# Kernel optimization log

Hardware: AMD Instinct MI355X
Metric: run time of the kernel (lower is better)

Reference implementation:

```python
import jax, jax.numpy as jnp
import numpy as np

B, S, H, L = 64, 512, 768, 9


def setup_inputs() -> dict:
    key = jax.random.key(0)
    ks = jax.random.split(key, 8)
    hidden = jax.random.normal(ks[0], (B, S, H), jnp.float32)
    lengths = jax.random.randint(ks[1], (B,), S // 2, S + 1)
    attention_mask = (jnp.arange(S)[None, :] < lengths[:, None]).astype(jnp.int32)
    labels = jax.random.randint(ks[2], (B, S), 0, L)
    # sprinkle some -100 ignore labels like HF datasets do
    ignore = jax.random.uniform(ks[3], (B, S)) < 0.05
    labels = jnp.where(ignore, -100, labels)
    W = jax.random.normal(ks[4], (H, L), jnp.float32) * 0.02
    b = jnp.zeros((L,), jnp.float32)
    start_transitions = jax.random.uniform(ks[5], (L,), jnp.float32, -0.1, 0.1)
    end_transitions = jax.random.uniform(ks[6], (L,), jnp.float32, -0.1, 0.1)
    transitions = jax.random.uniform(ks[7], (L, L), jnp.float32, -0.1, 0.1)
    return dict(hidden=hidden, attention_mask=attention_mask, labels=labels, W=W, b=b,
                start_transitions=start_transitions, end_transitions=end_transitions,
                transitions=transitions)


def _crf_numerator(emissions, tags, maskf, start_t, end_t, trans):
    # score of the gold tag sequence (torchcrf _compute_score)
    first = start_t[tags[:, 0]] + jnp.take_along_axis(emissions[:, 0], tags[:, 0:1], axis=1)[:, 0]
    em = jnp.take_along_axis(emissions, tags[..., None], axis=2)[..., 0]      # [B,S]
    tr = trans[tags[:, :-1], tags[:, 1:]]                                     # [B,S-1]
    score = first + jnp.sum((em[:, 1:] + tr) * maskf[:, 1:], axis=1)
    last_idx = (jnp.sum(maskf, axis=1).astype(jnp.int32) - 1)
    last_tags = jnp.take_along_axis(tags, last_idx[:, None], axis=1)[:, 0]
    return score + end_t[last_tags]


def _crf_lognorm(emissions, maskf, start_t, end_t, trans):
    # forward algorithm (torchcrf _compute_normalizer) as a lax.scan
    score0 = start_t[None, :] + emissions[:, 0]                               # [B,L]
    em_seq = jnp.transpose(emissions[:, 1:], (1, 0, 2))                       # [S-1,B,L]
    m_seq = maskf[:, 1:].T                                                    # [S-1,B]

    def step(score, xs):
        em_t, m_t = xs
        nxt = jax.nn.logsumexp(score[:, :, None] + trans[None] + em_t[:, None, :], axis=1)
        return jnp.where(m_t[:, None] > 0, nxt, score), None

    score, _ = jax.lax.scan(step, score0, (em_seq, m_seq))
    return jax.nn.logsumexp(score + end_t[None, :], axis=1)


def _viterbi(emissions, maskf, start_t, end_t, trans):
    score0 = start_t[None, :] + emissions[:, 0]                               # [B,L]
    em_seq = jnp.transpose(emissions[:, 1:], (1, 0, 2))
    m_seq = maskf[:, 1:].T

    def step(score, xs):
        em_t, m_t = xs
        cand = score[:, :, None] + trans[None]                                # [B,L,L]
        bp = jnp.argmax(cand, axis=1)                                         # [B,L]
        nxt = jnp.max(cand, axis=1) + em_t
        return jnp.where(m_t[:, None] > 0, nxt, score), bp

    score, history = jax.lax.scan(step, score0, (em_seq, m_seq))              # history [S-1,B,L]
    best_last = jnp.argmax(score + end_t[None, :], axis=1)                    # [B]

    def back(cur, xs):
        bp_t, m_t = xs
        prev = jnp.where(m_t > 0, jnp.take_along_axis(bp_t, cur[:, None], axis=1)[:, 0], cur)
        return prev, prev

    _, tags_rev = jax.lax.scan(back, best_last, (history[::-1], m_seq[::-1]))
    tags = jnp.concatenate([tags_rev[::-1].T, best_last[:, None]], axis=1)    # [B,S]
    return tags


def reference(hidden, attention_mask, labels, W, b, start_transitions, end_transitions, transitions):
    maskf = attention_mask.astype(hidden.dtype)                               # [B,S]
    logits = jnp.einsum('bsh,hl->bsl', hidden, W) + b                         # [B,S,L]
    safe_labels = jnp.where(labels == -100, 0, labels)
    num = _crf_numerator(logits, safe_labels, maskf, start_transitions, end_transitions, transitions)
    den = _crf_lognorm(logits, maskf, start_transitions, end_transitions, transitions)
    loss = -jnp.mean(num - den)                                               # -crf(..., reduction='mean')
    tags = _viterbi(logits, maskf, start_transitions, end_transitions, transitions)
    fake_logits = jax.nn.one_hot(tags, L, dtype=logits.dtype) * maskf[..., None]
    return loss, fake_logits
```

## Files before the change

### kernel.cpp

```cpp
#include <hip/hip_runtime.h>
#include <hip/hip_bf16.h>
#include <stdint.h>

constexpr int BB  = 64;
constexpr int SS  = 512;
constexpr int HH  = 768;
constexpr int NL  = 9;
constexpr int NROWS = BB * SS;
constexpr int EMN   = SS * NL;
constexpr int NSEG  = 8;
constexpr int NCH   = BB * NSEG * NL;
constexpr int GPW   = 7;
constexpr int NLOGW = (NCH + GPW - 1) / GPW;
constexpr float NEG  = -1e30f;

__device__ __forceinline__ float readlane_f(float v, int lane) {
  union { float f; int i; } u;
  u.f = v;
  u.i = __builtin_amdgcn_readlane(u.i, lane);
  return u.f;
}

__device__ __forceinline__ float bperm_f(int byte_addr, float v) {
  union { float f; int i; } u;
  u.f = v;
  u.i = __builtin_amdgcn_ds_bpermute(byte_addr, u.i);
  return u.f;
}

__device__ __forceinline__ float max3f(float a, float b, float c) {
  float d;
  asm("v_max3_f32 %0, %1, %2, %3" : "=v"(d) : "v"(a), "v"(b), "v"(c));
  return d;
}

__device__ __forceinline__ float max9f(const float* c) {
  return max3f(max3f(c[0], c[1], c[2]),
               max3f(c[3], c[4], c[5]),
               max3f(c[6], c[7], c[8]));
}

__global__ __launch_bounds__(256, 4) void logits_kernel(
    const float* __restrict__ hidden, const float* __restrict__ W,
    const float* __restrict__ bias, const int* __restrict__ mask,
    float* __restrict__ logits, int* __restrict__ lens,
    float* __restrict__ out, int* __restrict__ cnt) {
  const int lane = threadIdx.x & 63;
  const int wid  = blockIdx.x * 4 + (threadIdx.x >> 6);

  if (blockIdx.x == 0 && threadIdx.x == 0) out[0] = 0.0f;
  if (blockIdx.x == 1 && threadIdx.x < BB) cnt[threadIdx.x] = 0;

  if (blockIdx.x < 64 && threadIdx.x < 64) {
    const int4* mp = (const int4*)(mask + blockIdx.x * SS);
    const int4 a = mp[threadIdx.x];
    const int4 c = mp[threadIdx.x + 64];
    int lsum = a.x + a.y + a.z + a.w + c.x + c.y + c.z + c.w;
#pragma unroll
    for (int off = 32; off >= 1; off >>= 1) lsum += __shfl_xor(lsum, off, 64);
    if (threadIdx.x == 0) lens[blockIdx.x] = lsum;
  }

  const float my_bias = (lane < NL) ? bias[lane] : 0.0f;

  const float4* hp[4];
#pragma unroll
  for (int r = 0; r < 4; ++r)
    hp[r] = (const float4*)(hidden + (size_t)(wid + r * 8192) * HH);

  float acc[4][NL];
#pragma unroll
  for (int r = 0; r < 4; ++r)
#pragma unroll
    for (int l = 0; l < NL; ++l) acc[r][l] = 0.0f;

#pragma unroll
  for (int j = 0; j < 3; ++j) {
    float w[4][NL];
#pragma unroll
    for (int k = 0; k < 4; ++k) {
      const int r = lane * 4 + j * 256 + k;
#pragma unroll
      for (int l = 0; l < NL; ++l) w[k][l] = W[r * NL + l];
    }
#pragma unroll
    for (int r = 0; r < 4; ++r) {
      const float4 h = hp[r][lane + j * 64];
#pragma unroll
      for (int l = 0; l < NL; ++l)
        acc[r][l] += h.x * w[0][l] + h.y * w[1][l] +
                     h.z * w[2][l] + h.w * w[3][l];
    }
  }
#pragma unroll
  for (int off = 32; off >= 1; off >>= 1)
#pragma unroll
    for (int r = 0; r < 4; ++r)
#pragma unroll
      for (int l = 0; l < NL; ++l)
        acc[r][l] += __shfl_xor(acc[r][l], off, 64);
  if (lane < NL) {
#pragma unroll
    for (int r = 0; r < 4; ++r) {
      float v = acc[r][0];
#pragma unroll
      for (int l = 1; l < NL; ++l) if (lane == l) v = acc[r][l];
      logits[(size_t)(wid + r * 8192) * NL + lane] = v + my_bias;
    }
  }
}

__device__ void combine_batch(int b, int tid,
                              const float* __restrict__ logits,
                              const float* __restrict__ segmat,
                              const float* __restrict__ start_t,
                              const float* __restrict__ end_t,
                              const float* __restrict__ num_den,
                              float* __restrict__ out) {
  const int j = (tid < NL) ? tid : NL - 1;
  float s[NL];
#pragma unroll
  for (int i = 0; i < NL; ++i) s[i] = start_t[i] + logits[(size_t)b * EMN + i];
  float mcur[NL], mnxt[NL];
  {
    const float* M = segmat + (size_t)(b * NSEG) * 81;
#pragma unroll
    for (int i = 0; i < NL; ++i) mcur[i] = M[i * NL + j];
  }
  for (int sg = 0; sg < NSEG; ++sg) {
    if (sg + 1 < NSEG) {
      const float* M = segmat + (size_t)(b * NSEG + sg + 1) * 81;
#pragma unroll
      for (int i = 0; i < NL; ++i) mnxt[i] = M[i * NL + j];
    }
    float c[NL];
#pragma unroll
    for (int i = 0; i < NL; ++i) c[i] = s[i] + mcur[i];
    const float m = max9f(c);
    float sum = 0.0f;
#pragma unroll
    for (int i = 0; i < NL; ++i) sum += __expf(c[i] - m);
    const float nxt = m + __logf(sum);
#pragma unroll
    for (int i = 0; i < NL; ++i) s[i] = readlane_f(nxt, i);
#pragma unroll
    for (int i = 0; i < NL; ++i) mcur[i] = mnxt[i];
  }
  float c[NL];
#pragma unroll
  for (int i = 0; i < NL; ++i) c[i] = s[i] + end_t[i];
  const float m = max9f(c);
  float sum = 0.0f;
#pragma unroll
  for (int i = 0; i < NL; ++i) sum += __expf(c[i] - m);
  if (tid == 0) {
    const float den = m + __logf(sum);
    atomicAdd(out, (den - num_den[b]) * (1.0f / 64.0f));
  }
}

__global__ __launch_bounds__(64) void scan_kernel(
    const float* __restrict__ logits, const int* __restrict__ labels,
    const float* __restrict__ start_t, const float* __restrict__ end_t,
    const float* __restrict__ trans, float* __restrict__ out,
    float* __restrict__ num_den, const int* __restrict__ lens,
    float* __restrict__ segmat, int* __restrict__ cnt) {
  __shared__ uint32_t bpw[64 * NL];
  __shared__ unsigned char tags_s[SS];
  __shared__ unsigned char lab[SS];

  const int blk = blockIdx.x;
  const int tid = threadIdx.x;
  const int j   = (tid < NL) ? tid : NL - 1;

  if (blk < 64) {
    __builtin_amdgcn_s_setprio(1);
    const int b   = blk;
    const int len = lens[b];
    const float* emb = logits + (size_t)b * EMN;

    float tc[NL];
#pragma unroll
    for (int i = 0; i < NL; ++i) tc[i] = trans[i * NL + j];
    float s[NL];
#pragma unroll
    for (int i = 0; i < NL; ++i) s[i] = start_t[i] + emb[i];

    float e0[8], e1[8];
#pragma unroll
    for (int k = 0; k < 8; ++k) e0[k] = emb[(1 + k) * NL + j];

    for (int tb = 0; tb < 64; ++tb) {
      const int tbase = 8 * tb;
      if (tbase + 1 >= len) break;
      if (tb < 63) {
#pragma unroll
        for (int k = 0; k < 8; ++k) e1[k] = emb[(tbase + 9 + k) * NL + j];
      }
      uint32_t wpk = 0;
#pragma unroll
      for (int k = 0; k < 8; ++k) {
        const int t = tbase + 1 + k;
        if (t < len) {
          float c[NL];
#pragma unroll
          for (int i = 0; i < NL; ++i) c[i] = s[i] + tc[i];
          const float best = max9f(c);
          const float nxt  = best + e0[k];
          {
            const bool b01 = c[0] >= c[1], b23 = c[2] >= c[3];
            const bool b45 = c[4] >= c[5], b67 = c[6] >= c[7];
            const float v01 = b01 ? c[0] : c[1]; const int i01 = b01 ? 0 : 1;
            const float v23 = b23 ? c[2] : c[3]; const int i23 = b23 ? 2 : 3;
            const float v45 = b45 ? c[4] : c[5]; const int i45 = b45 ? 4 : 5;
            const float v67 = b67 ? c[6] : c[7]; const int i67 = b67 ? 6 : 7;
            const bool bA = v01 >= v23, bB = v45 >= v67;
            const float vA = bA ? v01 : v23; const int iA = bA ? i01 : i23;
            const float vB = bB ? v45 : v67; const int iB = bB ? i45 : i67;
            const bool bC = vA >= vB;
            const float vC = bC ? vA : vB; const int iC = bC ? iA : iB;
            const bool bD = vC >= c[8];
            const int arg = bD ? iC : 8;
            wpk |= (uint32_t)arg << (4 * k);
          }
#pragma unroll
          for (int i = 0; i < NL; ++i) s[i] = readlane_f(nxt, i);
        }
      }
      if (tid < NL) bpw[tb * NL + tid] = wpk;
#pragma unroll
      for (int k = 0; k < 8; ++k) e0[k] = e1[k];
    }
    float bv = s[0] + end_t[0];
    int   bl = 0;
#pragma unroll
    for (int i = 1; i < NL; ++i) {
      const float cc = s[i] + end_t[i];
      if (cc > bv) { bv = cc; bl = i; }
    }
    __syncthreads();

    uint32_t wv_[NL];
#pragma unroll
    for (int x = 0; x < NL; ++x) wv_[x] = bpw[tid * NL + x];
    uint64_t C = 0x876543210ULL;
#pragma unroll
    for (int k = 1; k <= 8; ++k) {
      const int t = 8 * tid + k;
      uint64_t nc = 0;
#pragma unroll
      for (int x = 0; x < 9; ++x) {
        const int g = (int)((wv_[x] >> (4 * (k - 1))) & 15u);
        nc |= ((C >> (4 * g)) & 15ULL) << (4 * x);
      }
      C = (t < len) ? nc : C;
    }
    const uint32_t Clo = (uint32_t)C, Chi = (uint32_t)(C >> 32);
    uint32_t cur = (uint32_t)bl;
    int bnd = 0;
#pragma unroll
    for (int c = 63; c >= 0; --c) {
      bnd = (tid == c) ? (int)cur : bnd;
      const uint32_t lo = (uint32_t)__builtin_amdgcn_readlane((int)Clo, c);
      const uint32_t hi = (uint32_t)__builtin_amdgcn_readlane((int)Chi, c);
      const uint64_t cc = ((uint64_t)hi << 32) | lo;
      cur = (uint32_t)((cc >> (4 * cur)) & 15u);
    }
    int tag = bnd;
#pragma unroll
    for (int k = 8; k >= 1; --k) {
      const int t = 8 * tid + k;
      const int tt = (t < 512) ? t : 511;
      const int blk2 = (tt - 1) >> 3;
      const int kk   = tt - 8 * blk2;
      const uint32_t bw = bpw[blk2 * NL + tag];
      const int nt = (int)((bw >> (4 * (kk - 1))) & 15u);
      tag = (t < len) ? nt : tag;
      tags_s[t - 1] = (unsigned char)tag;
    }
    __syncthreads();
    for (int i = tid; i < EMN; i += 64) {
      const int t = i / NL;
      const int l = i - t * NL;
      out[1 + (size_t)b * EMN + i] =
          (t < len && l == (int)tags_s[t]) ? 1.0f : 0.0f;
    }

  } else if (blk < 128) {
    const int b   = blk - 64;
    const int len = lens[b];
    const float* emb = logits + (size_t)b * EMN;
    for (int t = tid; t < SS; t += 64) {
      const int v = labels[b * SS + t];
      lab[t] = (unsigned char)((v == -100) ? 0 : v);
    }
    __syncthreads();
    float contrib = 0.0f;
    for (int t = tid; t < SS; t += 64) {
      if (t >= 1 && t < len)
        contrib += emb[t * NL + lab[t]] + trans[lab[t - 1] * NL + lab[t]];
    }
#pragma unroll
    for (int off = 32; off >= 1; off >>= 1)
      contrib += __shfl_xor(contrib, off, 64);
    if (tid == 0) {
      const int l0 = lab[0];
      num_den[b] = start_t[l0] + emb[l0] + contrib + end_t[lab[len - 1]];
    }
    __threadfence();
    int old = -1;
    if (tid == 0) old = atomicAdd(&cnt[b], 1);
    old = __builtin_amdgcn_readlane(old, 0);
    if (old == 72) {
      __threadfence();
      combine_batch(b, tid, logits, segmat, start_t, end_t, num_den, out);
    }

  } else {
    const int w   = blk - 128;
    const int g   = tid / 9;
    const int i   = tid - 9 * g;
    const int cid = GPW * w + g;
    const bool valid = (g < GPW) && (cid < NCH);
    const int cc  = valid ? cid : (NCH - 1);
    const int pr  = cc / 9;
    const int e   = cc - 9 * pr;
    const int b   = pr >> 3;
    const int sg  = pr & 7;
    const int len = lens[b];
    const int base4 = (g < GPW) ? (9 * g * 4) : 0;
    const float* embp = logits + (size_t)b * EMN + i;

    float tc[NL];
#pragma unroll
    for (int k = 0; k < NL; ++k) tc[k] = trans[k * NL + i];
    float my = (i == e) ? 0.0f : NEG;
    const int tbeg = 64 * sg + 1;

    float eA = embp[(size_t)(tbeg    ) * NL], eB = embp[(size_t)(tbeg + 1) * NL];
    float eC = embp[(size_t)(tbeg + 2) * NL], eD = embp[(size_t)(tbeg + 3) * NL];

    for (int st = 0; st < 64; ++st) {
      const int t = tbeg + st;
      if (__ballot((g < GPW) && (t < len)) == 0ull) break;
      float s[NL], c[NL];
#pragma unroll
      for (int k = 0; k < NL; ++k) s[k] = bperm_f(base4 + 4 * k, my);
#pragma unroll
      for (int k = 0; k < NL; ++k) c[k] = s[k] + tc[k];
      const float m = max9f(c);
      float u = 0.0f;
#pragma unroll
      for (int k = 0; k < NL; ++k) u += __expf(c[k] - m);
      const float nv = m + __logf(u) + eA;
      my = (t < len) ? nv : my;
      eA = eB; eB = eC; eC = eD;
      eD = embp[(size_t)(t + 4) * NL];
    }
    if (valid) segmat[(size_t)pr * 81 + e * NL + i] = my;
    __threadfence();
    int old = -1;
    if (valid && i == 0) old = atomicAdd(&cnt[b], 1);
#pragma unroll
    for (int g2 = 0; g2 < GPW; ++g2) {
      const int og = __builtin_amdgcn_readlane(old, 9 * g2);
      if (og == 72) {
        const int bg = __builtin_amdgcn_readlane(b, 9 * g2);
        __threadfence();
        combine_batch(bg, tid, logits, segmat, start_t, end_t, num_den, out);
      }
    }
  }
}

extern "C" void kernel_launch(void* const* d_in, const int* in_sizes, int n_in,
                              void* d_out, int out_size, void* d_ws, size_t ws_size,
                              hipStream_t stream) {
  const float* hidden  = (const float*)d_in[0];
  const int*   mask    = (const int*)d_in[1];
  const int*   labels  = (const int*)d_in[2];
  const float* W       = (const float*)d_in[3];
  const float* bias    = (const float*)d_in[4];
  const float* start_t = (const float*)d_in[5];
  const float* end_t   = (const float*)d_in[6];
  const float* trans   = (const float*)d_in[7];
  float* out = (float*)d_out;

  float* logits  = (float*)d_ws;
  float* segmat  = logits + (size_t)NROWS * NL;
  float* num_den = segmat + (size_t)BB * NSEG * 81;
  int*   lens    = (int*)(num_den + 128);
  int*   cnt     = lens + 64;

  logits_kernel<<<2048, 256, 0, stream>>>(hidden, W, bias, mask, logits, lens,
                                          out, cnt);
  scan_kernel<<<128 + NLOGW, 64, 0, stream>>>(logits, labels, start_t, end_t,
                                              trans, out, num_den, lens,
                                              segmat, cnt);
}
```

Baseline: 251.0 us.

## Interleave two length-sorted Viterbi chains per wave with LDS-staged emissions

Each Viterbi block now processes two batch rows whose lengths are adjacent in sorted order, interleaving their serial recurrences so the independent dependency chains hide each other's latency. Emissions for both rows are preloaded into shared memory, and the per-step broadcast switches from readlane to ds_swizzle. This halves the number of Viterbi blocks. In exchange it raises register and LDS pressure, adds a rank computation at the start, and makes each block's serial path as long as its longer row.

```diff
diff --git a/kernel.cpp b/kernel.cpp
--- a/kernel.cpp
+++ b/kernel.cpp
@@ -28,6 +28,19 @@
   return u.f;
 }
 
+#define SWZ_BCAST(dst, src, I)                                        \
+  { union { float f; int i; } _u; _u.f = (src);                       \
+    _u.i = __builtin_amdgcn_ds_swizzle(_u.i, ((I) << 5));             \
+    (dst) = _u.f; }
+
+__device__ __forceinline__ void swz_bcast9(float* s, float nxt) {
+  SWZ_BCAST(s[0], nxt, 0); SWZ_BCAST(s[1], nxt, 1);
+  SWZ_BCAST(s[2], nxt, 2); SWZ_BCAST(s[3], nxt, 3);
+  SWZ_BCAST(s[4], nxt, 4); SWZ_BCAST(s[5], nxt, 5);
+  SWZ_BCAST(s[6], nxt, 6); SWZ_BCAST(s[7], nxt, 7);
+  SWZ_BCAST(s[8], nxt, 8);
+}
+
 __device__ __forceinline__ float max3f(float a, float b, float c) {
   float d;
   asm("v_max3_f32 %0, %1, %2, %3" : "=v"(d) : "v"(a), "v"(b), "v"(c));
@@ -38,6 +51,22 @@
   return max3f(max3f(c[0], c[1], c[2]),
                max3f(c[3], c[4], c[5]),
                max3f(c[6], c[7], c[8]));
+}
+
+__device__ __forceinline__ int arg9(const float* c) {
+  const bool b01 = c[0] >= c[1], b23 = c[2] >= c[3];
+  const bool b45 = c[4] >= c[5], b67 = c[6] >= c[7];
+  const float v01 = b01 ? c[0] : c[1]; const int i01 = b01 ? 0 : 1;
+  const float v23 = b23 ? c[2] : c[3]; const int i23 = b23 ? 2 : 3;
+  const float v45 = b45 ? c[4] : c[5]; const int i45 = b45 ? 4 : 5;
+  const float v67 = b67 ? c[6] : c[7]; const int i67 = b67 ? 6 : 7;
+  const bool bA = v01 >= v23, bB = v45 >= v67;
+  const float vA = bA ? v01 : v23; const int iA = bA ? i01 : i23;
+  const float vB = bB ? v45 : v67; const int iB = bB ? i45 : i67;
+  const bool bC = vA >= vB;
+  const float vC = bC ? vA : vB; const int iC = bC ? iA : iB;
+  const bool bD = vC >= c[8];
+  return bD ? iC : 8;
 }
 
 __global__ __launch_bounds__(256, 4) void logits_kernel(
@@ -165,7 +194,10 @@
     const float* __restrict__ trans, float* __restrict__ out,
     float* __restrict__ num_den, const int* __restrict__ lens,
     float* __restrict__ segmat, int* __restrict__ cnt) {
-  __shared__ uint32_t bpw[64 * NL];
+  __shared__ float4   embvA[1161];
+  __shared__ float4   embvB[1161];
+  __shared__ uint32_t bpwA[64 * NL];
+  __shared__ uint32_t bpwB[64 * NL];
   __shared__ unsigned char tags_s[SS];
   __shared__ unsigned char lab[SS];
 
@@ -173,121 +205,189 @@
   const int tid = threadIdx.x;
   const int j   = (tid < NL) ? tid : NL - 1;
 
-  if (blk < 64) {
+  if (blk < 32) {
     __builtin_amdgcn_s_setprio(1);
-    const int b   = blk;
-    const int len = lens[b];
-    const float* emb = logits + (size_t)b * EMN;
+    const int lenv = lens[tid];
+    int rank = 0;
+    for (int c2 = 0; c2 < 64; ++c2) {
+      const int lc = __shfl(lenv, c2, 64);
+      rank += (lc < lenv || (lc == lenv && c2 < tid)) ? 1 : 0;
+    }
+    const unsigned long long mA = __ballot(rank == 2 * blk);
+    const unsigned long long mB = __ballot(rank == 2 * blk + 1);
+    const int bA = __ffsll(mA) - 1;
+    const int bB = __ffsll(mB) - 1;
+    const int lenA = __shfl(lenv, bA, 64);
+    const int lenB = __shfl(lenv, bB, 64);
+    const float* embA = logits + (size_t)bA * EMN;
+    const float* embB = logits + (size_t)bB * EMN;
+
+    {
+      const float4* a4 = (const float4*)embA;
+      const float4* b4 = (const float4*)embB;
+#pragma unroll
+      for (int i = 0; i < 18; ++i) {
+        embvA[tid + i * 64] = a4[tid + i * 64];
+        embvB[tid + i * 64] = b4[tid + i * 64];
+      }
+    }
+    __syncthreads();
+    const float* emb_sA = (const float*)embvA;
+    const float* emb_sB = (const float*)embvB;
 
     float tc[NL];
 #pragma unroll
     for (int i = 0; i < NL; ++i) tc[i] = trans[i * NL + j];
-    float s[NL];
-#pragma unroll
-    for (int i = 0; i < NL; ++i) s[i] = start_t[i] + emb[i];
-
-    float e0[8], e1[8];
-#pragma unroll
-    for (int k = 0; k < 8; ++k) e0[k] = emb[(1 + k) * NL + j];
-
-    for (int tb = 0; tb < 64; ++tb) {
+    float sA[NL], sB[NL];
+#pragma unroll
+    for (int i = 0; i < NL; ++i) {
+      sA[i] = start_t[i] + emb_sA[i];
+      sB[i] = start_t[i] + emb_sB[i];
+    }
+
+    float e0A[8], e1A[8], e0B[8], e1B[8];
+#pragma unroll
+    for (int k = 0; k < 8; ++k) {
+      e0A[k] = emb_sA[(1 + k) * NL + j];
+      e0B[k] = emb_sB[(1 + k) * NL + j];
+    }
+
+    const int minlen = (lenA < lenB) ? lenA : lenB;
+    const int nfmin  = (minlen - 1) >> 3;
+
+    for (int tb = 0; tb < nfmin; ++tb) {
       const int tbase = 8 * tb;
-      if (tbase + 1 >= len) break;
-      if (tb < 63) {
-#pragma unroll
-        for (int k = 0; k < 8; ++k) e1[k] = emb[(tbase + 9 + k) * NL + j];
-      }
-      uint32_t wpk = 0;
 #pragma unroll
       for (int k = 0; k < 8; ++k) {
-        const int t = tbase + 1 + k;
-        if (t < len) {
+        e1A[k] = emb_sA[(tbase + 9 + k) * NL + j];
+        e1B[k] = emb_sB[(tbase + 9 + k) * NL + j];
+      }
+      uint32_t wA = 0, wB = 0;
+#pragma unroll
+      for (int k = 0; k < 8; ++k) {
+        {
           float c[NL];
 #pragma unroll
-          for (int i = 0; i < NL; ++i) c[i] = s[i] + tc[i];
+          for (int i = 0; i < NL; ++i) c[i] = sA[i] + tc[i];
           const float best = max9f(c);
-          const float nxt  = best + e0[k];
-          {
-            const bool b01 = c[0] >= c[1], b23 = c[2] >= c[3];
-            const bool b45 = c[4] >= c[5], b67 = c[6] >= c[7];
-            const float v01 = b01 ? c[0] : c[1]; const int i01 = b01 ? 0 : 1;
-            const float v23 = b23 ? c[2] : c[3]; const int i23 = b23 ? 2 : 3;
-            const float v45 = b45 ? c[4] : c[5]; const int i45 = b45 ? 4 : 5;
-            const float v67 = b67 ? c[6] : c[7]; const int i67 = b67 ? 6 : 7;
-            const bool bA = v01 >= v23, bB = v45 >= v67;
-            const float vA = bA ? v01 : v23; const int iA = bA ? i01 : i23;
-            const float vB = bB ? v45 : v67; const int iB = bB ? i45 : i67;
-            const bool bC = vA >= vB;
-            const float vC = bC ? vA : vB; const int iC = bC ? iA : iB;
-            const bool bD = vC >= c[8];
-            const int arg = bD ? iC : 8;
-            wpk |= (uint32_t)arg << (4 * k);
-          }
-#pragma unroll
-          for (int i = 0; i < NL; ++i) s[i] = readlane_f(nxt, i);
+          const float nxt  = best + e0A[k];
+          swz_bcast9(sA, nxt);
+          wA |= (uint32_t)arg9(c) << (4 * k);
         }
-      }
-      if (tid < NL) bpw[tb * NL + tid] = wpk;
-#pragma unroll
-      for (int k = 0; k < 8; ++k) e0[k] = e1[k];
-    }
-    float bv = s[0] + end_t[0];
-    int   bl = 0;
-#pragma unroll
-    for (int i = 1; i < NL; ++i) {
-      const float cc = s[i] + end_t[i];
-      if (cc > bv) { bv = cc; bl = i; }
+        {
+          float c[NL];
+#pragma unroll
+          for (int i = 0; i < NL; ++i) c[i] = sB[i] + tc[i];
+          const float best = max9f(c);
+          const float nxt  = best + e0B[k];
+          swz_bcast9(sB, nxt);
+          wB |= (uint32_t)arg9(c) << (4 * k);
+        }
+      }
+      if (tid < NL) { bpwA[tb * NL + tid] = wA; bpwB[tb * NL + tid] = wB; }
+#pragma unroll
+      for (int k = 0; k < 8; ++k) { e0A[k] = e1A[k]; e0B[k] = e1B[k]; }
+    }
+    for (int tb = nfmin; tb < 64; ++tb) {
+      const int t0 = 8 * tb + 1;
+      if (t0 >= lenA && t0 >= lenB) break;
+      uint32_t wA = 0, wB = 0;
+#pragma unroll
+      for (int k = 0; k < 8; ++k) {
+        const int t = t0 + k;
+        if (t < lenA) {
+          const float e = emb_sA[t * NL + j];
+          float c[NL];
+#pragma unroll
+          for (int i = 0; i < NL; ++i) c[i] = sA[i] + tc[i];
+          const float best = max9f(c);
+          const float nxt  = best + e;
+          swz_bcast9(sA, nxt);
+          wA |= (uint32_t)arg9(c) << (4 * k);
+        }
+        if (t < lenB) {
+          const float e = emb_sB[t * NL + j];
+          float c[NL];
+#pragma unroll
+          for (int i = 0; i < NL; ++i) c[i] = sB[i] + tc[i];
+          const float best = max9f(c);
+          const float nxt  = best + e;
+          swz_bcast9(sB, nxt);
+          wB |= (uint32_t)arg9(c) << (4 * k);
+        }
+      }
+      if (tid < NL) { bpwA[tb * NL + tid] = wA; bpwB[tb * NL + tid] = wB; }
+    }
+#pragma unroll
+    for (int i = 0; i < NL; ++i) {
+      sA[i] = readlane_f(sA[i], 0);
+      sB[i] = readlane_f(sB[i], 0);
     }
     __syncthreads();
 
-    uint32_t wv_[NL];
-#pragma unroll
-    for (int x = 0; x < NL; ++x) wv_[x] = bpw[tid * NL + x];
-    uint64_t C = 0x876543210ULL;
-#pragma unroll
-    for (int k = 1; k <= 8; ++k) {
-      const int t = 8 * tid + k;
-      uint64_t nc = 0;
-#pragma unroll
-      for (int x = 0; x < 9; ++x) {
-        const int g = (int)((wv_[x] >> (4 * (k - 1))) & 15u);
-        nc |= ((C >> (4 * g)) & 15ULL) << (4 * x);
-      }
-      C = (t < len) ? nc : C;
-    }
-    const uint32_t Clo = (uint32_t)C, Chi = (uint32_t)(C >> 32);
-    uint32_t cur = (uint32_t)bl;
-    int bnd = 0;
-#pragma unroll
-    for (int c = 63; c >= 0; --c) {
-      bnd = (tid == c) ? (int)cur : bnd;
-      const uint32_t lo = (uint32_t)__builtin_amdgcn_readlane((int)Clo, c);
-      const uint32_t hi = (uint32_t)__builtin_amdgcn_readlane((int)Chi, c);
-      const uint64_t cc = ((uint64_t)hi << 32) | lo;
-      cur = (uint32_t)((cc >> (4 * cur)) & 15u);
-    }
-    int tag = bnd;
-#pragma unroll
-    for (int k = 8; k >= 1; --k) {
-      const int t = 8 * tid + k;
-      const int tt = (t < 512) ? t : 511;
-      const int blk2 = (tt - 1) >> 3;
-      const int kk   = tt - 8 * blk2;
-      const uint32_t bw = bpw[blk2 * NL + tag];
-      const int nt = (int)((bw >> (4 * (kk - 1))) & 15u);
-      tag = (t < len) ? nt : tag;
-      tags_s[t - 1] = (unsigned char)tag;
-    }
-    __syncthreads();
-    for (int i = tid; i < EMN; i += 64) {
-      const int t = i / NL;
-      const int l = i - t * NL;
-      out[1 + (size_t)b * EMN + i] =
-          (t < len && l == (int)tags_s[t]) ? 1.0f : 0.0f;
-    }
-
-  } else if (blk < 128) {
-    const int b   = blk - 64;
+    for (int ch = 0; ch < 2; ++ch) {
+      const uint32_t* bp = (ch == 0) ? bpwA : bpwB;
+      const float*    sv = (ch == 0) ? sA : sB;
+      const int       ln = (ch == 0) ? lenA : lenB;
+      const int       bb = (ch == 0) ? bA : bB;
+
+      float bv = sv[0] + end_t[0];
+      int   bl = 0;
+#pragma unroll
+      for (int i = 1; i < NL; ++i) {
+        const float cc = sv[i] + end_t[i];
+        if (cc > bv) { bv = cc; bl = i; }
+      }
+      uint32_t wv_[NL];
+#pragma unroll
+      for (int x = 0; x < NL; ++x) wv_[x] = bp[tid * NL + x];
+      uint64_t C = 0x876543210ULL;
+#pragma unroll
+      for (int k = 1; k <= 8; ++k) {
+        const int t = 8 * tid + k;
+        uint64_t nc = 0;
+#pragma unroll
+        for (int x = 0; x < 9; ++x) {
+          const int g = (int)((wv_[x] >> (4 * (k - 1))) & 15u);
+          nc |= ((C >> (4 * g)) & 15ULL) << (4 * x);
+        }
+        C = (t < ln) ? nc : C;
+      }
+      const uint32_t Clo = (uint32_t)C, Chi = (uint32_t)(C >> 32);
+      uint32_t cur = (uint32_t)bl;
+      int bnd = 0;
+#pragma unroll
+      for (int c = 63; c >= 0; --c) {
+        bnd = (tid == c) ? (int)cur : bnd;
+        const uint32_t lo = (uint32_t)__builtin_amdgcn_readlane((int)Clo, c);
+        const uint32_t hi = (uint32_t)__builtin_amdgcn_readlane((int)Chi, c);
+        const uint64_t cc = ((uint64_t)hi << 32) | lo;
+        cur = (uint32_t)((cc >> (4 * cur)) & 15u);
+      }
+      int tag = bnd;
+#pragma unroll
+      for (int k = 8; k >= 1; --k) {
+        const int t = 8 * tid + k;
+        const int tt = (t < 512) ? t : 511;
+        const int blk2 = (tt - 1) >> 3;
+        const int kk   = tt - 8 * blk2;
+        const uint32_t bw = bp[blk2 * NL + tag];
+        const int nt = (int)((bw >> (4 * (kk - 1))) & 15u);
+        tag = (t < ln) ? nt : tag;
+        tags_s[t - 1] = (unsigned char)tag;
+      }
+      __syncthreads();
+      for (int i = tid; i < EMN; i += 64) {
+        const int t = i / NL;
+        const int l = i - t * NL;
+        out[1 + (size_t)bb * EMN + i] =
+            (t < ln && l == (int)tags_s[t]) ? 1.0f : 0.0f;
+      }
+      __syncthreads();
+    }
+
+  } else if (blk < 96) {
+    const int b   = blk - 32;
     const int len = lens[b];
     const float* emb = logits + (size_t)b * EMN;
     for (int t = tid; t < SS; t += 64) {
@@ -317,7 +417,7 @@
     }
 
   } else {
-    const int w   = blk - 128;
+    const int w   = blk - 96;
     const int g   = tid / 9;
     const int i   = tid - 9 * g;
     const int cid = GPW * w + g;
@@ -394,7 +494,7 @@
 
   logits_kernel<<<2048, 256, 0, stream>>>(hidden, W, bias, mask, logits, lens,
                                           out, cnt);
-  scan_kernel<<<128 + NLOGW, 64, 0, stream>>>(logits, labels, start_t, end_t,
-                                              trans, out, num_den, lens,
-                                              segmat, cnt);
-}
+  scan_kernel<<<96 + NLOGW, 64, 0, stream>>>(logits, labels, start_t, end_t,
+                                             trans, out, num_den, lens,
+                                             segmat, cnt);
+}
```

After: 302.2 us. 1.2x slower.

## Compute Viterbi recurrence redundantly per lane and defer backpointer argmax to parallel pass

Applied to the files above, without the earlier changes.

The Viterbi forward loop no longer gives each lane one tag column and broadcasts scores with readlane. Every lane now computes all nine max-plus columns from a register-held transition matrix, using emissions staged once into shared memory. It records the score trajectory to shared memory, and a later parallel pass spread over 63 lanes recomputes the argmax backpointers. The aim is to take the cross-lane readlane latency and the argmax logic off the serial 511-step dependency chain. In exchange, each step does about nine times more redundant VALU work, uses more registers and uses more LDS.

```diff
diff --git a/kernel.cpp b/kernel.cpp
--- a/kernel.cpp
+++ b/kernel.cpp
@@ -40,6 +40,22 @@
                max3f(c[6], c[7], c[8]));
 }
 
+__device__ __forceinline__ int arg9(const float* c) {
+  const bool b01 = c[0] >= c[1], b23 = c[2] >= c[3];
+  const bool b45 = c[4] >= c[5], b67 = c[6] >= c[7];
+  const float v01 = b01 ? c[0] : c[1]; const int i01 = b01 ? 0 : 1;
+  const float v23 = b23 ? c[2] : c[3]; const int i23 = b23 ? 2 : 3;
+  const float v45 = b45 ? c[4] : c[5]; const int i45 = b45 ? 4 : 5;
+  const float v67 = b67 ? c[6] : c[7]; const int i67 = b67 ? 6 : 7;
+  const bool bA = v01 >= v23, bB = v45 >= v67;
+  const float vA = bA ? v01 : v23; const int iA = bA ? i01 : i23;
+  const float vB = bB ? v45 : v67; const int iB = bB ? i45 : i67;
+  const bool bC = vA >= vB;
+  const float vC = bC ? vA : vB; const int iC = bC ? iA : iB;
+  const bool bD = vC >= c[8];
+  return bD ? iC : 8;
+}
+
 __global__ __launch_bounds__(256, 4) void logits_kernel(
     const float* __restrict__ hidden, const float* __restrict__ W,
     const float* __restrict__ bias, const int* __restrict__ mask,
@@ -165,8 +181,10 @@
     const float* __restrict__ trans, float* __restrict__ out,
     float* __restrict__ num_den, const int* __restrict__ lens,
     float* __restrict__ segmat, int* __restrict__ cnt) {
-  __shared__ uint32_t bpw[64 * NL];
-  __shared__ unsigned char tags_s[SS];
+  __shared__ float4   embv[1161];
+  __shared__ float    straj[SS * NL];
+  __shared__ unsigned char bp_s[EMN];
+  __shared__ uint32_t tags_w[64];
   __shared__ unsigned char lab[SS];
 
   const int blk = blockIdx.x;
@@ -179,57 +197,51 @@
     const int len = lens[b];
     const float* emb = logits + (size_t)b * EMN;
 
-    float tc[NL];
-#pragma unroll
-    for (int i = 0; i < NL; ++i) tc[i] = trans[i * NL + j];
+    {
+      const float4* src = (const float4*)emb;
+#pragma unroll
+      for (int i = 0; i < 18; ++i) embv[tid + i * 64] = src[tid + i * 64];
+    }
+    __syncthreads();
+    const float* emb_s = (const float*)embv;
+
+    float tcA[NL][NL];
+#pragma unroll
+    for (int i = 0; i < NL; ++i)
+#pragma unroll
+      for (int jj = 0; jj < NL; ++jj) tcA[i][jj] = trans[i * NL + jj];
+
     float s[NL];
 #pragma unroll
-    for (int i = 0; i < NL; ++i) s[i] = start_t[i] + emb[i];
-
-    float e0[8], e1[8];
-#pragma unroll
-    for (int k = 0; k < 8; ++k) e0[k] = emb[(1 + k) * NL + j];
-
-    for (int tb = 0; tb < 64; ++tb) {
-      const int tbase = 8 * tb;
-      if (tbase + 1 >= len) break;
-      if (tb < 63) {
-#pragma unroll
-        for (int k = 0; k < 8; ++k) e1[k] = emb[(tbase + 9 + k) * NL + j];
+    for (int i = 0; i < NL; ++i) s[i] = start_t[i] + emb_s[i];
+    {
+      float w = s[0];
+#pragma unroll
+      for (int jj = 1; jj < NL; ++jj) w = (tid == jj) ? s[jj] : w;
+      if (tid < NL) straj[tid] = w;
+    }
+
+    float e_cur[NL], e_nxt[NL];
+#pragma unroll
+    for (int i = 0; i < NL; ++i) e_cur[i] = emb_s[1 * NL + i];
+
+    for (int t = 1; t < len; ++t) {
+#pragma unroll
+      for (int i = 0; i < NL; ++i) e_nxt[i] = emb_s[(t + 1) * NL + i];
+      float nxt[NL];
+      float w = 0.0f;
+#pragma unroll
+      for (int jj = 0; jj < NL; ++jj) {
+        float c[NL];
+#pragma unroll
+        for (int i = 0; i < NL; ++i) c[i] = s[i] + tcA[i][jj];
+        const float best = max9f(c);
+        nxt[jj] = best + e_cur[jj];
+        w = (jj == 0) ? nxt[0] : ((tid == jj) ? nxt[jj] : w);
       }
-      uint32_t wpk = 0;
-#pragma unroll
-      for (int k = 0; k < 8; ++k) {
-        const int t = tbase + 1 + k;
-        if (t < len) {
-          float c[NL];
-#pragma unroll
-          for (int i = 0; i < NL; ++i) c[i] = s[i] + tc[i];
-          const float best = max9f(c);
-          const float nxt  = best + e0[k];
-          {
-            const bool b01 = c[0] >= c[1], b23 = c[2] >= c[3];
-            const bool b45 = c[4] >= c[5], b67 = c[6] >= c[7];
-            const float v01 = b01 ? c[0] : c[1]; const int i01 = b01 ? 0 : 1;
-            const float v23 = b23 ? c[2] : c[3]; const int i23 = b23 ? 2 : 3;
-            const float v45 = b45 ? c[4] : c[5]; const int i45 = b45 ? 4 : 5;
-            const float v67 = b67 ? c[6] : c[7]; const int i67 = b67 ? 6 : 7;
-            const bool bA = v01 >= v23, bB = v45 >= v67;
-            const float vA = bA ? v01 : v23; const int iA = bA ? i01 : i23;
-            const float vB = bB ? v45 : v67; const int iB = bB ? i45 : i67;
-            const bool bC = vA >= vB;
-            const float vC = bC ? vA : vB; const int iC = bC ? iA : iB;
-            const bool bD = vC >= c[8];
-            const int arg = bD ? iC : 8;
-            wpk |= (uint32_t)arg << (4 * k);
-          }
-#pragma unroll
-          for (int i = 0; i < NL; ++i) s[i] = readlane_f(nxt, i);
-        }
-      }
-      if (tid < NL) bpw[tb * NL + tid] = wpk;
-#pragma unroll
-      for (int k = 0; k < 8; ++k) e0[k] = e1[k];
+      if (tid < NL) straj[t * NL + tid] = w;
+#pragma unroll
+      for (int i = 0; i < NL; ++i) { s[i] = nxt[i]; e_cur[i] = e_nxt[i]; }
     }
     float bv = s[0] + end_t[0];
     int   bl = 0;
@@ -240,18 +252,36 @@
     }
     __syncthreads();
 
-    uint32_t wv_[NL];
-#pragma unroll
-    for (int x = 0; x < NL; ++x) wv_[x] = bpw[tid * NL + x];
+    {
+      const int g  = tid / 9;
+      const int jj = tid - 9 * g;
+      if (g < 7) {
+        float tcol[NL];
+#pragma unroll
+        for (int i = 0; i < NL; ++i) tcol[i] = trans[i * NL + jj];
+        for (int tt = 0; tt < 73; ++tt) {
+          const int t = 1 + g + 7 * tt;
+          if (t < len) {
+            float c[NL];
+#pragma unroll
+            for (int i = 0; i < NL; ++i) c[i] = straj[(t - 1) * NL + i] + tcol[i];
+            bp_s[t * NL + jj] = (unsigned char)arg9(c);
+          }
+        }
+      }
+    }
+    __syncthreads();
+
     uint64_t C = 0x876543210ULL;
 #pragma unroll
     for (int k = 1; k <= 8; ++k) {
-      const int t = 8 * tid + k;
+      const int t  = 8 * tid + k;
+      const int ti = (t < 512) ? t : 511;
       uint64_t nc = 0;
 #pragma unroll
       for (int x = 0; x < 9; ++x) {
-        const int g = (int)((wv_[x] >> (4 * (k - 1))) & 15u);
-        nc |= ((C >> (4 * g)) & 15ULL) << (4 * x);
+        const int g2 = bp_s[ti * NL + x] & 15;
+        nc |= ((C >> (4 * g2)) & 15ULL) << (4 * x);
       }
       C = (t < len) ? nc : C;
     }
@@ -267,23 +297,22 @@
       cur = (uint32_t)((cc >> (4 * cur)) & 15u);
     }
     int tag = bnd;
+    uint32_t tw = 0;
 #pragma unroll
     for (int k = 8; k >= 1; --k) {
-      const int t = 8 * tid + k;
-      const int tt = (t < 512) ? t : 511;
-      const int blk2 = (tt - 1) >> 3;
-      const int kk   = tt - 8 * blk2;
-      const uint32_t bw = bpw[blk2 * NL + tag];
-      const int nt = (int)((bw >> (4 * (kk - 1))) & 15u);
+      const int t  = 8 * tid + k;
+      const int ti = (t < 512) ? t : 511;
+      const int nt = bp_s[ti * NL + tag];
       tag = (t < len) ? nt : tag;
-      tags_s[t - 1] = (unsigned char)tag;
-    }
+      tw |= (uint32_t)tag << (4 * (k - 1));
+    }
+    tags_w[tid] = tw;
     __syncthreads();
     for (int i = tid; i < EMN; i += 64) {
       const int t = i / NL;
       const int l = i - t * NL;
-      out[1 + (size_t)b * EMN + i] =
-          (t < len && l == (int)tags_s[t]) ? 1.0f : 0.0f;
+      const int tg = (int)((tags_w[t >> 3] >> ((t & 7) * 4)) & 15u);
+      out[1 + (size_t)b * EMN + i] = (t < len && l == tg) ? 1.0f : 0.0f;
     }
 
   } else if (blk < 128) {
```

Result: slower. 358.0 us (+42.6%).
